# Optimization experiments

Hardware: AMD Instinct MI355X
Metric: run time of the kernel (lower is better)

Reference implementation:

```python
import jax, jax.numpy as jnp
import numpy as np
import math

EMBED_DIM = 768
NUM_HEADS = 12
HEAD_DIM = EMBED_DIM // NUM_HEADS
R = 16
LORA_ALPHA = 16
SCALING = LORA_ALPHA / math.sqrt(R)  # 4.0
U = 1.0  # ramp_up_steps=0 -> u()=1.0


def lora_linear(x, W, b, A):
    # base F.linear + SingLoRA delta: delta_W = A @ A.T (symmetric)
    base = x @ W.T + b
    delta_W = A @ A.T  # [D, D]
    return base + (x @ delta_W.T) * (U * SCALING)


def setup_inputs() -> dict:
    key = jax.random.key(0)
    ks = jax.random.split(key, 16)
    B, S, D = 2, 2048, EMBED_DIM
    inv = 1.0 / math.sqrt(D)
    d = {
        'query': jax.random.normal(ks[0], (B, S, D), jnp.float32),
        'key': jax.random.normal(ks[1], (B, S, D), jnp.float32),
        'value': jax.random.normal(ks[2], (B, S, D), jnp.float32),
        'Wq': jax.random.normal(ks[3], (D, D), jnp.float32) * inv,
        'bq': jax.random.normal(ks[4], (D,), jnp.float32) * 0.01,
        'Aq': jax.random.normal(ks[5], (D, R), jnp.float32) * 0.01,
        'Wk': jax.random.normal(ks[6], (D, D), jnp.float32) * inv,
        'bk': jax.random.normal(ks[7], (D,), jnp.float32) * 0.01,
        'Ak': jax.random.normal(ks[8], (D, R), jnp.float32) * 0.01,
        'Wv': jax.random.normal(ks[9], (D, D), jnp.float32) * inv,
        'bv': jax.random.normal(ks[10], (D,), jnp.float32) * 0.01,
        'Av': jax.random.normal(ks[11], (D, R), jnp.float32) * 0.01,
        'Wo': jax.random.normal(ks[12], (D, D), jnp.float32) * inv,
        'bo': jax.random.normal(ks[13], (D,), jnp.float32) * 0.01,
    }
    return d


def reference(query, key, value, Wq, bq, Aq, Wk, bk, Ak, Wv, bv, Av, Wo, bo):
    B, S, D = query.shape
    H, hd = NUM_HEADS, HEAD_DIM
    q = lora_linear(query, Wq, bq, Aq)
    k = lora_linear(key, Wk, bk, Ak)
    v = lora_linear(value, Wv, bv, Av)
    # [B, S, D] -> [B, H, S, hd]
    q = q.reshape(B, S, H, hd).transpose(0, 2, 1, 3)
    k = k.reshape(B, S, H, hd).transpose(0, 2, 1, 3)
    v = v.reshape(B, S, H, hd).transpose(0, 2, 1, 3)
    scores = jnp.einsum('bhqd,bhkd->bhqk', q, k) / math.sqrt(hd)
    attn = jax.nn.softmax(scores, axis=-1)
    out = jnp.einsum('bhqk,bhkd->bhqd', attn, v)  # [B, H, S, hd]
    out = out.transpose(0, 2, 1, 3).reshape(B, S, D)
    out = out @ Wo.T + bo
    return out
```

## Files before the change

### kernel.cpp

```cpp
#include <hip/hip_runtime.h>
#include <math.h>
#include <stdint.h>

#define D 768
#define S 2048
#define B_ 2
#define NROWS 4096
#define H 12
#define HD 64
#define R_ 16

typedef _Float16 half_t;
typedef _Float16 half8 __attribute__((ext_vector_type(8)));
typedef _Float16 half4 __attribute__((ext_vector_type(4)));
typedef float floatx4 __attribute__((ext_vector_type(4)));

#define MFMA32(a, b, c) __builtin_amdgcn_mfma_f32_16x16x32_f16(a, b, c, 0, 0, 0)
#define MFMA16(a, b, c) __builtin_amdgcn_mfma_f32_16x16x16f16(a, b, c, 0, 0, 0)
#define EXP2F(x) __builtin_amdgcn_exp2f(x)

#define SWAIT(N) __builtin_amdgcn_s_waitcnt(0x0F70 | (N))
#define SBAR() __builtin_amdgcn_s_barrier()

__device__ __forceinline__ void gl_lds16(const void* gp, half_t* lp) {
  __builtin_amdgcn_global_load_lds(
      (const __attribute__((address_space(1))) void*)(gp),
      (__attribute__((address_space(3))) void*)(lp), 16, 0, 0);
}


__global__ __launch_bounds__(256) void prep_kernel(
    const float* __restrict__ q, const float* __restrict__ k,
    const float* __restrict__ v, half_t* __restrict__ xq,
    half_t* __restrict__ xk, half_t* __restrict__ xv,
    const float* __restrict__ Wq, const float* __restrict__ Aq,
    const float* __restrict__ Wk, const float* __restrict__ Ak,
    const float* __restrict__ Wv, const float* __restrict__ Av,
    const float* __restrict__ Wo, half_t* __restrict__ Mq,
    half_t* __restrict__ Mk, half_t* __restrict__ Mv,
    half_t* __restrict__ Mo) {
  const int bid = blockIdx.x;
  if (bid < 9216) {
    const int y = bid / 3072;
    const float* x = (y == 0) ? q : (y == 1) ? k : v;
    half_t* o = (y == 0) ? xq : (y == 1) ? xk : xv;
    int i = (bid - y * 3072) * 1024 + threadIdx.x * 4;
    float4 vv = *reinterpret_cast<const float4*>(x + i);
    half_t tmp[4] = {(half_t)vv.x, (half_t)vv.y, (half_t)vv.z, (half_t)vv.w};
    *reinterpret_cast<uint64_t*>(o + i) = *reinterpret_cast<uint64_t*>(tmp);
  } else {
    const int u = bid - 9216;
    const int y = u / 2304;
    const float* W = (y == 0) ? Wq : (y == 1) ? Wk : (y == 2) ? Wv : Wo;
    const float* A = (y == 0) ? Aq : (y == 1) ? Ak : (y == 2) ? Av : nullptr;
    half_t* M = (y == 0) ? Mq : (y == 1) ? Mk : (y == 2) ? Mv : Mo;
    int idx = (u - y * 2304) * 256 + threadIdx.x;
    int j = idx / D;
    int kk = idx - j * D;
    float acc = W[idx];
    if (A != nullptr) {
      float s = 0.f;
#pragma unroll
      for (int r = 0; r < R_; ++r) s += A[kk * R_ + r] * A[j * R_ + r];
      acc += 4.0f * s;
    }
    M[idx] = (half_t)acc;
  }
}

__global__ __launch_bounds__(256) void gemm_qkv_kernel(
    const half_t* __restrict__ x0, const half_t* __restrict__ x1,
    const half_t* __restrict__ x2, const half_t* __restrict__ m0,
    const half_t* __restrict__ m1, const half_t* __restrict__ m2,
    const float* __restrict__ b0, const float* __restrict__ b1,
    const float* __restrict__ b2, half_t* __restrict__ o0,
    half_t* __restrict__ o1, half_t* __restrict__ o2) {
  constexpr int AG = 16;
  constexpr int G = AG + 16;
  constexpr int PB = G * 512;
  __shared__ __align__(16) half_t smem[2 * PB];

  const int z = blockIdx.z;
  const half_t* X = (z == 0) ? x0 : (z == 1) ? x1 : x2;
  const half_t* M = (z == 0) ? m0 : (z == 1) ? m1 : m2;
  const float* bias = (z == 0) ? b0 : (z == 1) ? b1 : b2;
  half_t* Out = (z == 0) ? o0 : (z == 1) ? o1 : o2;

  const int tid = threadIdx.x;
  const int lane = tid & 63;
  const int wv = tid >> 6;
  const int lr = lane & 15;
  const int lq = lane >> 4;
  const int row0 = blockIdx.y * 128;
  const int j0 = blockIdx.x * 128;
  const int wr = wv >> 1;
  const int wc = wv & 1;

  floatx4 acc[4][4] = {};

#define GSTAGE(bufi, k0)                                                       \
  do {                                                                         \
    _Pragma("unroll") for (int gi = 0; gi < 8; ++gi) {                         \
      int g = wv * 8 + gi;                                                     \
      if (g < AG) {                                                            \
        int t = g >> 1, c = g & 1;                                             \
        gl_lds16(                                                              \
            X + (size_t)(row0 + t * 16 + lr) * D + (k0) + c * 32 + lq * 8,     \
            smem + (bufi)*PB + g * 512);                                       \
      } else {                                                                 \
        int g2 = g - AG;                                                       \
        int u = g2 >> 1, c = g2 & 1;                                           \
        gl_lds16(                                                              \
            M + (size_t)(j0 + u * 16 + lr) * D + (k0) + c * 32 + lq * 8,       \
            smem + (bufi)*PB + AG * 512 + g2 * 512);                           \
      }                                                                        \
    }                                                                          \
  } while (0)

  GSTAGE(0, 0);
  __syncthreads();

  for (int it = 0; it < D / 64; ++it) {
    const int cur = it & 1;
    if (it + 1 < D / 64) GSTAGE(cur ^ 1, (it + 1) * 64);
    const half_t* Ab = smem + cur * PB;
    const half_t* Bb = Ab + AG * 512;
#pragma unroll
    for (int c = 0; c < 2; ++c) {
      half8 af[4], bf[4];
#pragma unroll
      for (int t = 0; t < 4; ++t)
        af[t] = *reinterpret_cast<const half8*>(
            &Ab[(((wr * 4 + t) * 2 + c) * 64 + lane) * 8]);
#pragma unroll
      for (int u = 0; u < 4; ++u)
        bf[u] = *reinterpret_cast<const half8*>(
            &Bb[(((wc * 4 + u) * 2 + c) * 64 + lane) * 8]);
#pragma unroll
      for (int t = 0; t < 4; ++t)
#pragma unroll
        for (int u = 0; u < 4; ++u) acc[t][u] = MFMA32(af[t], bf[u], acc[t][u]);
    }
    __syncthreads();
  }
#undef GSTAGE

  float bv[4];
#pragma unroll
  for (int u = 0; u < 4; ++u) bv[u] = bias[j0 + (wc * 4 + u) * 16 + lr];

  if (z == 2) {
    const int bb = row0 >> 11;
    const int kb0 = (row0 & 2047) >> 6;
#pragma unroll
    for (int t = 0; t < 4; ++t) {
#pragma unroll
      for (int u = 0; u < 4; ++u) {
        int gc = j0 + (wc * 4 + u) * 16 + lr;
        int hh = gc >> 6;
        int ud = (gc & 63) >> 4;
        half4 hv;
#pragma unroll
        for (int r = 0; r < 4; ++r) hv[r] = (half_t)(acc[t][u][r] + bv[u]);
        size_t addr = ((size_t)(bb * H + hh) * HD) * S +
                      (size_t)(kb0 + wr) * 4096 +
                      (ud * 2 + ((t >> 1) & 1)) * 512 + lane * 8 + (t & 1) * 4;
        *reinterpret_cast<half4*>(&Out[addr]) = hv;
      }
    }
    return;
  }

#pragma unroll
  for (int t = 0; t < 4; ++t) {
#pragma unroll
    for (int u = 0; u < 4; ++u) {
#pragma unroll
      for (int r = 0; r < 4; ++r) {
        int gr = row0 + (wr * 4 + t) * 16 + lq * 4 + r;
        int gc = j0 + (wc * 4 + u) * 16 + lr;
        Out[(size_t)gr * D + gc] = (half_t)(acc[t][u][r] + bv[u]);
      }
    }
  }
}

__global__ __launch_bounds__(256) void gemm_o_kernel(
    const half_t* __restrict__ Xh, const half_t* __restrict__ M,
    const float* __restrict__ bias, float* __restrict__ Out) {
  constexpr int AG = 8;
  constexpr int G = 16;
  constexpr int PB = G * 512;
  __shared__ __align__(16) half_t smem[3 * PB];

  const int tid = threadIdx.x;
  const int lane = tid & 63;
  const int wv = tid >> 6;
  const int lr = lane & 15;
  const int lq = lane >> 4;
  const int row0 = blockIdx.y * 64;
  const int j0 = blockIdx.x * 64;
  const int wr = wv >> 1;
  const int wc = wv & 1;

  floatx4 acc[2][2] = {};

#define GSTAGE(soff, k0)                                                       \
  do {                                                                         \
    _Pragma("unroll") for (int gi = 0; gi < 4; ++gi) {                         \
      int g = wv * 4 + gi;                                                     \
      if (g < AG) {                                                            \
        int t = g >> 1, c = g & 1;                                             \
        gl_lds16(                                                              \
            Xh + (size_t)(row0 + t * 16 + lr) * D + (k0) + c * 32 + lq * 8,    \
            smem + (soff) + g * 512);                                          \
      } else {                                                                 \
        int g2 = g - AG;                                                       \
        int u = g2 >> 1, c = g2 & 1;                                           \
        gl_lds16(                                                              \
            M + (size_t)(j0 + u * 16 + lr) * D + (k0) + c * 32 + lq * 8,       \
            smem + (soff) + AG * 512 + g2 * 512);                              \
      }                                                                        \
    }                                                                          \
  } while (0)

  GSTAGE(0, 0);
  GSTAGE(PB, 64);
  SWAIT(4);
  SBAR();

  int co = 0, so = 2 * PB;
  for (int it = 0; it < D / 64; ++it) {
    if (it + 2 < D / 64) GSTAGE(so, (it + 2) * 64);
    const half_t* Ab = smem + co;
    const half_t* Bb = Ab + AG * 512;
#pragma unroll
    for (int c = 0; c < 2; ++c) {
      half8 af[2], bf[2];
#pragma unroll
      for (int t = 0; t < 2; ++t)
        af[t] = *reinterpret_cast<const half8*>(
            &Ab[(((wr * 2 + t) * 2 + c) * 64 + lane) * 8]);
#pragma unroll
      for (int u = 0; u < 2; ++u)
        bf[u] = *reinterpret_cast<const half8*>(
            &Bb[(((wc * 2 + u) * 2 + c) * 64 + lane) * 8]);
#pragma unroll
      for (int t = 0; t < 2; ++t)
#pragma unroll
        for (int u = 0; u < 2; ++u) acc[t][u] = MFMA32(af[t], bf[u], acc[t][u]);
    }
    if (it + 2 < D / 64) SWAIT(4); else SWAIT(0);
    SBAR();
    co += PB; if (co == 3 * PB) co = 0;
    so += PB; if (so == 3 * PB) so = 0;
  }
#undef GSTAGE

  float bv[2];
#pragma unroll
  for (int u = 0; u < 2; ++u) bv[u] = bias[j0 + (wc * 2 + u) * 16 + lr];
#pragma unroll
  for (int t = 0; t < 2; ++t) {
#pragma unroll
    for (int u = 0; u < 2; ++u) {
#pragma unroll
      for (int r = 0; r < 4; ++r) {
        int gr = row0 + (wr * 2 + t) * 16 + lq * 4 + r;
        int gc = j0 + (wc * 2 + u) * 16 + lr;
        Out[(size_t)gr * D + gc] = acc[t][u][r] + bv[u];
      }
    }
  }
}

__global__ __launch_bounds__(512, 6) void attn_mfma_kernel(
    const half_t* __restrict__ Qh, const half_t* __restrict__ Kh,
    const half_t* __restrict__ Vt2, half_t* __restrict__ Oh) {
  __shared__ __align__(16) half_t smem[24576];
  half_t* Ks = smem;
  half_t* Vs = smem + 12288;

  const int tid = threadIdx.x;
  const int lane = tid & 63;
  const int wv = tid >> 6;
  const int t_ = wv & 3;
  const int half_ = wv >> 2;
  const int lr = lane & 15;
  const int lq = lane >> 4;
  const int q0 = blockIdx.x * 64;
  const int h = blockIdx.y;
  const int b = blockIdx.z;
  const size_t base = (size_t)b * S * D + h * HD;
  const size_t vtbase = (size_t)(b * H + h) * HD * (size_t)S;
  const int qw = q0 + t_ * 16;

  const half_t qscale = (half_t)0.18033688f;
  half8 qf[2];
#pragma unroll
  for (int c = 0; c < 2; ++c) {
    half8 qv = *reinterpret_cast<const half8*>(
        &Qh[base + (size_t)(qw + lr) * D + c * 32 + lq * 8]);
#pragma unroll
    for (int j = 0; j < 8; ++j) qv[j] = qv[j] * qscale;
    qf[c] = qv;
  }

  half4 ones;
#pragma unroll
  for (int j = 0; j < 4; ++j) ones[j] = (half_t)1.0f;

  floatx4 o[4] = {};
  floatx4 ol = {};

#define STAGE(soff, kb)                                                        \
  do {                                                                         \
    _Pragma("unroll") for (int gi = 0; gi < 2; ++gi) {                         \
      int g = wv * 2 + gi;                                                     \
      if (g < 8) {                                                             \
        int u = g >> 1, c = g & 1;                                             \
        gl_lds16(                                                              \
            Kh + base + (size_t)((kb) + u * 16 + lr) * D + c * 32 + lq * 8,    \
            Ks + (soff) + g * 512);                                            \
      } else {                                                                 \
        int gv = g - 8;                                                        \
        gl_lds16(Vt2 + vtbase + (size_t)(kb)*64 + gv * 512 + lane * 8,         \
                 Vs + (soff) + gv * 512);                                      \
      }                                                                        \
    }                                                                          \
  } while (0)

  STAGE(0, 0);
  STAGE(4096, 64);
  SWAIT(2);
  SBAR();

  int co = 0, so = 8192;
  for (int it = 0; it < S / 64; ++it) {
    if (it + 2 < S / 64) STAGE(so, (it + 2) * 64);

    half4 pf[2];
#pragma unroll
    for (int ui = 0; ui < 2; ++ui) {
      const int u = half_ * 2 + ui;
      half8 kf0 = *reinterpret_cast<const half8*>(
          &Ks[co + ((u * 2 + 0) * 64 + lane) * 8]);
      half8 kf1 = *reinterpret_cast<const half8*>(
          &Ks[co + ((u * 2 + 1) * 64 + lane) * 8]);
      floatx4 st = {};
      st = MFMA32(kf0, qf[0], st);
      st = MFMA32(kf1, qf[1], st);
      pf[ui][0] = (half_t)EXP2F(st[0]);
      pf[ui][1] = (half_t)EXP2F(st[1]);
      pf[ui][2] = (half_t)EXP2F(st[2]);
      pf[ui][3] = (half_t)EXP2F(st[3]);
    }
#pragma unroll
    for (int ud = 0; ud < 4; ++ud) {
      half8 vf8 = *reinterpret_cast<const half8*>(
          &Vs[co + ((ud * 2 + half_) * 64 + lane) * 8]);
      half4 vlo, vhi;
#pragma unroll
      for (int j = 0; j < 4; ++j) {
        vlo[j] = vf8[j];
        vhi[j] = vf8[4 + j];
      }
      o[ud] = MFMA16(pf[0], vlo, o[ud]);
      o[ud] = MFMA16(pf[1], vhi, o[ud]);
    }
    ol = MFMA16(pf[0], ones, ol);
    ol = MFMA16(pf[1], ones, ol);

    if (it + 2 < S / 64) SWAIT(2); else SWAIT(0);
    SBAR();
    co += 4096; if (co == 12288) co = 0;
    so += 4096; if (so == 12288) so = 0;
  }
#undef STAGE

  float* red = (float*)smem;
  const int slot = t_ * 64 + lane;
  if (half_ == 1) {
#pragma unroll
    for (int comp = 0; comp < 16; ++comp)
      red[comp * 260 + slot] = o[comp >> 2][comp & 3];
#pragma unroll
    for (int r = 0; r < 4; ++r) red[(16 + r) * 260 + slot] = ol[r];
  }
  __syncthreads();
  if (half_ == 0) {
#pragma unroll
    for (int comp = 0; comp < 16; ++comp)
      o[comp >> 2][comp & 3] += red[comp * 260 + slot];
    float linv[4];
#pragma unroll
    for (int r = 0; r < 4; ++r)
      linv[r] = 1.0f / (ol[r] + red[(16 + r) * 260 + slot]);
#pragma unroll
    for (int ud = 0; ud < 4; ++ud) {
#pragma unroll
      for (int r = 0; r < 4; ++r) {
        int row = qw + lq * 4 + r;
        int col = h * HD + ud * 16 + lr;
        Oh[(size_t)(b * S + row) * D + col] = (half_t)(o[ud][r] * linv[r]);
      }
    }
  }
}

extern "C" void kernel_launch(void* const* d_in, const int* in_sizes, int n_in,
                              void* d_out, int out_size, void* d_ws,
                              size_t ws_size, hipStream_t stream) {
  const float* query = (const float*)d_in[0];
  const float* key   = (const float*)d_in[1];
  const float* value = (const float*)d_in[2];
  const float* Wq = (const float*)d_in[3];
  const float* bq = (const float*)d_in[4];
  const float* Aq = (const float*)d_in[5];
  const float* Wk = (const float*)d_in[6];
  const float* bk = (const float*)d_in[7];
  const float* Ak = (const float*)d_in[8];
  const float* Wv = (const float*)d_in[9];
  const float* bv = (const float*)d_in[10];
  const float* Av = (const float*)d_in[11];
  const float* Wo = (const float*)d_in[12];
  const float* bo = (const float*)d_in[13];
  float* out = (float*)d_out;

  half_t* hw = (half_t*)d_ws;
  const size_t XSZ = (size_t)NROWS * D;
  const size_t MSZ = (size_t)D * D;
  half_t* xq = hw;
  half_t* xk = xq + XSZ;
  half_t* xv = xk + XSZ;
  half_t* qh = xv + XSZ;
  half_t* kh = qh + XSZ;
  half_t* vt = kh + XSZ;
  half_t* ab = vt + XSZ;
  half_t* Mq = ab + XSZ;
  half_t* Mk = Mq + MSZ;
  half_t* Mv = Mk + MSZ;
  half_t* Mo = Mv + MSZ;

  prep_kernel<<<18432, 256, 0, stream>>>(query, key, value, xq, xk, xv, Wq, Aq,
                                         Wk, Ak, Wv, Av, Wo, Mq, Mk, Mv, Mo);

  dim3 gq(D / 128, NROWS / 128, 3);
  gemm_qkv_kernel<<<gq, 256, 0, stream>>>(xq, xk, xv, Mq, Mk, Mv, bq, bk, bv,
                                          qh, kh, vt);

  dim3 ga(S / 64, H, B_);
  attn_mfma_kernel<<<ga, 512, 0, stream>>>(qh, kh, vt, ab);

  dim3 go(D / 64, NROWS / 64, 1);
  gemm_o_kernel<<<go, 256, 0, stream>>>(ab, Mo, bo, out);
}
```

Before: 217.0 us.

## Triple-buffer QKV GEMM, swizzle block order, merge PV MFMAs to 16x16x32

The QKV GEMM moves from double-buffered 64-wide K steps to a three-stage ring of 32-wide K steps, with waitcnt-based barriers in place of __syncthreads. All three kernels remap the linear block index with a stride-8 swizzle so that consecutively scheduled blocks spread across different tiles, which is meant to improve L2 locality. In attention, each pair of 16x16x16 MFMAs for PV and the row sum is replaced by one 16x16x32 MFMA on a concatenated half8, so fewer instructions issue. The risks are a shorter per-stage compute window in the GEMM and a possible mismatch in K-index pairing between the packed P fragment and the V layout.

```diff
diff --git a/kernel.cpp b/kernel.cpp
--- a/kernel.cpp
+++ b/kernel.cpp
@@ -16,7 +16,6 @@
 typedef float floatx4 __attribute__((ext_vector_type(4)));
 
 #define MFMA32(a, b, c) __builtin_amdgcn_mfma_f32_16x16x32_f16(a, b, c, 0, 0, 0)
-#define MFMA16(a, b, c) __builtin_amdgcn_mfma_f32_16x16x16f16(a, b, c, 0, 0, 0)
 #define EXP2F(x) __builtin_amdgcn_exp2f(x)
 
 #define SWAIT(N) __builtin_amdgcn_s_waitcnt(0x0F70 | (N))
@@ -75,12 +74,18 @@
     const float* __restrict__ b0, const float* __restrict__ b1,
     const float* __restrict__ b2, half_t* __restrict__ o0,
     half_t* __restrict__ o1, half_t* __restrict__ o2) {
-  constexpr int AG = 16;
-  constexpr int G = AG + 16;
+  constexpr int AG = 8;
+  constexpr int G = 16;
   constexpr int PB = G * 512;
-  __shared__ __align__(16) half_t smem[2 * PB];
-
-  const int z = blockIdx.z;
+  __shared__ __align__(16) half_t smem[3 * PB];
+
+  int lin = blockIdx.x + 6 * (blockIdx.y + 32 * blockIdx.z);
+  lin = (lin & 7) * 72 + (lin >> 3);
+  const int z = lin / 192;
+  const int rem = lin - z * 192;
+  const int by = rem / 6;
+  const int bx = rem - by * 6;
+
   const half_t* X = (z == 0) ? x0 : (z == 1) ? x1 : x2;
   const half_t* M = (z == 0) ? m0 : (z == 1) ? m1 : m2;
   const float* bias = (z == 0) ? b0 : (z == 1) ? b1 : b2;
@@ -91,57 +96,54 @@
   const int wv = tid >> 6;
   const int lr = lane & 15;
   const int lq = lane >> 4;
-  const int row0 = blockIdx.y * 128;
-  const int j0 = blockIdx.x * 128;
+  const int row0 = by * 128;
+  const int j0 = bx * 128;
   const int wr = wv >> 1;
   const int wc = wv & 1;
 
   floatx4 acc[4][4] = {};
 
-#define GSTAGE(bufi, k0)                                                       \
-  do {                                                                         \
-    _Pragma("unroll") for (int gi = 0; gi < 8; ++gi) {                         \
-      int g = wv * 8 + gi;                                                     \
-      if (g < AG) {                                                            \
-        int t = g >> 1, c = g & 1;                                             \
-        gl_lds16(                                                              \
-            X + (size_t)(row0 + t * 16 + lr) * D + (k0) + c * 32 + lq * 8,     \
-            smem + (bufi)*PB + g * 512);                                       \
-      } else {                                                                 \
-        int g2 = g - AG;                                                       \
-        int u = g2 >> 1, c = g2 & 1;                                           \
-        gl_lds16(                                                              \
-            M + (size_t)(j0 + u * 16 + lr) * D + (k0) + c * 32 + lq * 8,       \
-            smem + (bufi)*PB + AG * 512 + g2 * 512);                           \
-      }                                                                        \
-    }                                                                          \
+#define GSTAGE(soff, k0)                                                      \
+  do {                                                                        \
+    _Pragma("unroll") for (int gi = 0; gi < 4; ++gi) {                        \
+      int g = wv * 4 + gi;                                                    \
+      if (g < AG) {                                                           \
+        gl_lds16(X + (size_t)(row0 + g * 16 + lr) * D + (k0) + lq * 8,        \
+                 smem + (soff) + g * 512);                                    \
+      } else {                                                                \
+        gl_lds16(M + (size_t)(j0 + (g - AG) * 16 + lr) * D + (k0) + lq * 8,   \
+                 smem + (soff) + g * 512);                                    \
+      }                                                                       \
+    }                                                                         \
   } while (0)
 
   GSTAGE(0, 0);
-  __syncthreads();
-
-  for (int it = 0; it < D / 64; ++it) {
-    const int cur = it & 1;
-    if (it + 1 < D / 64) GSTAGE(cur ^ 1, (it + 1) * 64);
-    const half_t* Ab = smem + cur * PB;
+  GSTAGE(PB, 32);
+  SWAIT(4);
+  SBAR();
+
+  int co = 0, so = 2 * PB;
+  for (int it = 0; it < D / 32; ++it) {
+    if (it + 2 < D / 32) GSTAGE(so, (it + 2) * 32);
+    const half_t* Ab = smem + co;
     const half_t* Bb = Ab + AG * 512;
-#pragma unroll
-    for (int c = 0; c < 2; ++c) {
-      half8 af[4], bf[4];
-#pragma unroll
-      for (int t = 0; t < 4; ++t)
-        af[t] = *reinterpret_cast<const half8*>(
-            &Ab[(((wr * 4 + t) * 2 + c) * 64 + lane) * 8]);
-#pragma unroll
-      for (int u = 0; u < 4; ++u)
-        bf[u] = *reinterpret_cast<const half8*>(
-            &Bb[(((wc * 4 + u) * 2 + c) * 64 + lane) * 8]);
-#pragma unroll
-      for (int t = 0; t < 4; ++t)
-#pragma unroll
-        for (int u = 0; u < 4; ++u) acc[t][u] = MFMA32(af[t], bf[u], acc[t][u]);
-    }
-    __syncthreads();
+    half8 af[4], bf[4];
+#pragma unroll
+    for (int t = 0; t < 4; ++t)
+      af[t] = *reinterpret_cast<const half8*>(
+          &Ab[((wr * 4 + t) * 64 + lane) * 8]);
+#pragma unroll
+    for (int u = 0; u < 4; ++u)
+      bf[u] = *reinterpret_cast<const half8*>(
+          &Bb[((wc * 4 + u) * 64 + lane) * 8]);
+#pragma unroll
+    for (int t = 0; t < 4; ++t)
+#pragma unroll
+      for (int u = 0; u < 4; ++u) acc[t][u] = MFMA32(af[t], bf[u], acc[t][u]);
+    if (it + 2 < D / 32) SWAIT(4); else SWAIT(0);
+    SBAR();
+    co += PB; if (co == 3 * PB) co = 0;
+    so += PB; if (so == 3 * PB) so = 0;
   }
 #undef GSTAGE
 
@@ -193,13 +195,18 @@
   constexpr int PB = G * 512;
   __shared__ __align__(16) half_t smem[3 * PB];
 
+  int lin = blockIdx.x + 12 * blockIdx.y;
+  lin = (lin & 7) * 96 + (lin >> 3);
+  const int bx = lin % 12;
+  const int byy = lin / 12;
+
   const int tid = threadIdx.x;
   const int lane = tid & 63;
   const int wv = tid >> 6;
   const int lr = lane & 15;
   const int lq = lane >> 4;
-  const int row0 = blockIdx.y * 64;
-  const int j0 = blockIdx.x * 64;
+  const int row0 = byy * 64;
+  const int j0 = bx * 64;
   const int wr = wv >> 1;
   const int wc = wv & 1;
 
@@ -288,9 +295,14 @@
   const int half_ = wv >> 2;
   const int lr = lane & 15;
   const int lq = lane >> 4;
-  const int q0 = blockIdx.x * 64;
-  const int h = blockIdx.y;
-  const int b = blockIdx.z;
+
+  int lin = blockIdx.x + 32 * (blockIdx.y + 12 * blockIdx.z);
+  lin = (lin & 7) * 96 + (lin >> 3);
+  const int q0 = (lin & 31) * 64;
+  const int hb = lin >> 5;
+  const int h = hb % 12;
+  const int b = hb / 12;
+
   const size_t base = (size_t)b * S * D + h * HD;
   const size_t vtbase = (size_t)(b * H + h) * HD * (size_t)S;
   const int qw = q0 + t_ * 16;
@@ -306,9 +318,9 @@
     qf[c] = qv;
   }
 
-  half4 ones;
-#pragma unroll
-  for (int j = 0; j < 4; ++j) ones[j] = (half_t)1.0f;
+  half8 ones8;
+#pragma unroll
+  for (int j = 0; j < 8; ++j) ones8[j] = (half_t)1.0f;
 
   floatx4 o[4] = {};
   floatx4 ol = {};
@@ -339,7 +351,7 @@
   for (int it = 0; it < S / 64; ++it) {
     if (it + 2 < S / 64) STAGE(so, (it + 2) * 64);
 
-    half4 pf[2];
+    half8 pv;
 #pragma unroll
     for (int ui = 0; ui < 2; ++ui) {
       const int u = half_ * 2 + ui;
@@ -350,26 +362,18 @@
       floatx4 st = {};
       st = MFMA32(kf0, qf[0], st);
       st = MFMA32(kf1, qf[1], st);
-      pf[ui][0] = (half_t)EXP2F(st[0]);
-      pf[ui][1] = (half_t)EXP2F(st[1]);
-      pf[ui][2] = (half_t)EXP2F(st[2]);
-      pf[ui][3] = (half_t)EXP2F(st[3]);
+      pv[4 * ui + 0] = (half_t)EXP2F(st[0]);
+      pv[4 * ui + 1] = (half_t)EXP2F(st[1]);
+      pv[4 * ui + 2] = (half_t)EXP2F(st[2]);
+      pv[4 * ui + 3] = (half_t)EXP2F(st[3]);
     }
 #pragma unroll
     for (int ud = 0; ud < 4; ++ud) {
       half8 vf8 = *reinterpret_cast<const half8*>(
           &Vs[co + ((ud * 2 + half_) * 64 + lane) * 8]);
-      half4 vlo, vhi;
-#pragma unroll
-      for (int j = 0; j < 4; ++j) {
-        vlo[j] = vf8[j];
-        vhi[j] = vf8[4 + j];
-      }
-      o[ud] = MFMA16(pf[0], vlo, o[ud]);
-      o[ud] = MFMA16(pf[1], vhi, o[ud]);
-    }
-    ol = MFMA16(pf[0], ones, ol);
-    ol = MFMA16(pf[1], ones, ol);
+      o[ud] = MFMA32(pv, vf8, o[ud]);
+    }
+    ol = MFMA32(pv, ones8, ol);
 
     if (it + 2 < S / 64) SWAIT(2); else SWAIT(0);
     SBAR();
```

Result: faster. 211.0 us (-2.8%).
